# Optimization experiments

Measured on AMD Instinct MI355X. Metric: run time of the kernel, lower is better.

The kernel has to match this reference:

```python
import jax, jax.numpy as jnp
from jax import lax
import numpy as np

N, D, H, ENT = 32768, 16, 128, 50000


def setup_inputs() -> dict:
    key = jax.random.key(0)
    ks = jax.random.split(key, 10)
    s = 0.05  # weight scale to keep tanh/sigmoid in active range
    return {
        "ent_table": jax.random.normal(ks[0], (ENT, H), jnp.float32) * s,
        "op_table": jax.random.normal(ks[1], (5, H), jnp.float32) * s,
        "non_table": jax.random.normal(ks[2], (1, H), jnp.float32) * s,
        "Wm": jax.random.normal(ks[3], (H, 3 * H), jnp.float32) * s,
        "bm": jnp.zeros((H,), jnp.float32),
        "Wg": jax.random.normal(ks[4], (H, 3 * H), jnp.float32) * s,
        "bg": jnp.zeros((H,), jnp.float32),
        "ops_idx": jax.random.randint(ks[5], (N, D), 0, 4, jnp.int32),
        "ents_idx": jax.random.randint(ks[6], (N, D + 1), 0, ENT, jnp.int32),
        "left_idx": jax.random.randint(ks[7], (N,), 0, ENT, jnp.int32),
    }


def reference(ent_table, op_table, non_table, Wm, bm, Wg, bg, ops_idx, ents_idx, left_idx):
    # Merge module (dropout in eval mode = identity):
    #   tanh(Linear([node, t1, t2])) * sigmoid(Linear_g([node, t1, t2]))
    def merge(node, t1, t2):
        x = jnp.concatenate([node, t1, t2], axis=-1)  # [N, 3H]
        return jnp.tanh(x @ Wm.T + bm) * jax.nn.sigmoid(x @ Wg.T + bg)

    op_e = op_table[ops_idx]        # [N, D, H]
    ent_e = ent_table[ents_idx]     # [N, D+1, H]

    # Right-leaning prefix tree: acc starts at deepest entity, merge upward.
    acc0 = ent_e[:, -1]             # [N, H]
    # scan over depth, from innermost (i = D-1) to outermost (i = 0)
    xs = (jnp.flip(op_e, axis=1).transpose(1, 0, 2),          # [D, N, H]
          jnp.flip(ent_e[:, :-1], axis=1).transpose(1, 0, 2))  # [D, N, H]

    def step(acc, inp):
        o, e = inp
        return merge(o, e, acc), None

    acc, _ = lax.scan(step, acc0, xs)

    eq_e = jnp.broadcast_to(op_table[4], acc.shape)  # '=' embedding, [N, H]
    left_e = ent_table[left_idx]                     # [N, H]
    score = merge(eq_e, left_e, acc)                 # [N, H]

    # all_score = cat(per-formula scores, non_embed)  -> [N+1, H]
    return jnp.concatenate([score, non_table], axis=0)
```

## Files before the change

kernel.cpp:

```cpp
#include <hip/hip_runtime.h>
#include <hip/hip_bf16.h>
#include <hip/hip_fp16.h>

#define NROWS 32768
#define HH 128
#define ENTN 50000

typedef _Float16 f16x8 __attribute__((ext_vector_type(8)));
typedef __fp16 fp16x2 __attribute__((ext_vector_type(2)));
typedef float f32x4 __attribute__((ext_vector_type(4)));
typedef float f32x16 __attribute__((ext_vector_type(16)));

#define OFF_PEB 0
#define OFF_EB  25600000
#define OFF_WF  38400000
#define OFF_PEF (OFF_WF + 65536)
#define OFF_POPK (OFF_PEF + 65536)

#define KM 2.8853901f
#define KG (-1.4426950f)
#define RSTR 272
#define HALF (32 * RSTR)

#if defined(__has_builtin)
#if __has_builtin(__builtin_amdgcn_exp2f)
#define FEXP2(x) __builtin_amdgcn_exp2f(x)
#endif
#endif
#ifndef FEXP2
__device__ __forceinline__ float __fexp2_asm(float x) {
    float r; asm("v_exp_f32 %0, %1" : "=v"(r) : "v"(x)); return r;
}
#define FEXP2(x) __fexp2_asm(x)
#endif

__device__ __forceinline__ unsigned pk2(float a, float b) {
    fp16x2 h = __builtin_amdgcn_cvt_pkrtz(a, b);
    unsigned u; __builtin_memcpy(&u, &h, 4); return u;
}
__device__ __forceinline__ unsigned pk2rtn(float a, float b) {
    _Float16 lo = (_Float16)a, hi = (_Float16)b;
    unsigned short ul, uh;
    __builtin_memcpy(&ul, &lo, 2); __builtin_memcpy(&uh, &hi, 2);
    return (unsigned)ul | ((unsigned)uh << 16);
}

__global__ void prep_kernel(const float* __restrict__ ent_table,
                            const float* __restrict__ op_table,
                            const float* __restrict__ non_table,
                            const float* __restrict__ Wm, const float* __restrict__ bm,
                            const float* __restrict__ Wg, const float* __restrict__ bg,
                            char* __restrict__ ws, float* __restrict__ out) {
    int idx = blockIdx.x * blockDim.x + threadIdx.x;
    if (idx < 800000) {
        _Float16* EB = (_Float16*)(ws + OFF_EB);
        int base = idx * 8;
        const float4* s = (const float4*)(ent_table + base);
        float4 v0 = s[0], v1 = s[1];
        float xv[8] = {v0.x, v0.y, v0.z, v0.w, v1.x, v1.y, v1.z, v1.w};
        _Float16 h8[8];
        #pragma unroll
        for (int j = 0; j < 8; ++j) h8[j] = (_Float16)xv[j];
        *(f16x8*)(EB + base) = *(f16x8*)h8;
    } else if (idx < 832768) {
        int e = idx - 800000;
        int jj = e & 7, l = (e >> 3) & 63, kt = (e >> 9) & 7, jb = e >> 12;
        int j = jb * 32 + (l & 31);
        int c = j >> 1, p = j & 1;
        int k = kt * 16 + (l >> 5) * 8 + jj;
        const float* Wrow = p ? (Wg + (size_t)c * 384) : (Wm + (size_t)c * 384);
        ((_Float16*)(ws + OFF_WF))[e] = (_Float16)(Wrow[256 + k] * (p ? KG : KM));
    } else if (idx < 865536) {
        int e = idx - 832768;
        int jj = e & 7, l = (e >> 3) & 63, kt = (e >> 9) & 3, jb = e >> 11;
        int j = jb * 16 + (l & 15);
        int c = j >> 1, p = j & 1;
        int k = kt * 32 + (l >> 4) * 8 + jj;
        const float* Wrow = p ? (Wg + (size_t)c * 384) : (Wm + (size_t)c * 384);
        ((_Float16*)(ws + OFF_PEF))[e] = (_Float16)Wrow[128 + k];
    } else if (idx < 866176) {
        int t2 = idx - 865536;
        int pr = t2 & 1, q = (t2 >> 1) & 3, h = (t2 >> 3) & 1, jb = (t2 >> 4) & 7, o = t2 >> 7;
        int j0 = jb * 32 + 8 * q + 4 * h + 2 * pr;
        int c = j0 >> 1;
        float sm = bm[c], sg = bg[c];
        const float* Wrm = Wm + (size_t)c * 384;
        const float* Wrg = Wg + (size_t)c * 384;
        for (int i = 0; i < 128; ++i) {
            float ov = op_table[o * HH + i];
            sm += ov * Wrm[i];
            sg += ov * Wrg[i];
        }
        ((unsigned*)(ws + OFF_POPK))[t2] = pk2rtn(sm * KM, sg * KG);
    } else if (idx < 866304) {
        int j = idx - 866176;
        out[(size_t)NROWS * HH + j] = non_table[j];
    }
}

__global__ __launch_bounds__(256, 4)
void pe_kernel(char* __restrict__ ws) {
    const char* EBc = ws + OFF_EB;
    const f16x8* PEF = (const f16x8*)(ws + OFF_PEF);
    char* PEB = ws + OFF_PEB;
    int tid = threadIdx.x, w = tid >> 6, l = tid & 63, lr = l & 15, lg = (l >> 4) & 3;
    int e0 = blockIdx.x * 32;

    f16x8 WB[4][4];
    #pragma unroll
    for (int u = 0; u < 4; ++u)
        #pragma unroll
        for (int kt = 0; kt < 4; ++kt)
            WB[u][kt] = PEF[((4 * w + u) * 4 + kt) * 64 + l];

    f32x4 C[2][4];
    #pragma unroll
    for (int rt = 0; rt < 2; ++rt)
        #pragma unroll
        for (int u = 0; u < 4; ++u) C[rt][u] = (f32x4){0.f, 0.f, 0.f, 0.f};

    #pragma unroll
    for (int kt = 0; kt < 4; ++kt) {
        #pragma unroll
        for (int rt = 0; rt < 2; ++rt) {
            int e = e0 + rt * 16 + lr;
            if (e >= ENTN) e = ENTN - 1;
            f16x8 A = *(const f16x8*)(EBc + (size_t)e * 256 + kt * 64 + lg * 16);
            #pragma unroll
            for (int u = 0; u < 4; ++u)
                C[rt][u] = __builtin_amdgcn_mfma_f32_16x16x32_f16(WB[u][kt], A, C[rt][u], 0, 0, 0);
        }
    }
    #pragma unroll
    for (int rt = 0; rt < 2; ++rt) {
        int e = e0 + rt * 16 + lr;
        if (e < ENTN) {
            #pragma unroll
            for (int u = 0; u < 4; ++u) {
                int c = (4 * w + u) * 8 + 2 * lg;
                int jb2 = c >> 4, rem = c & 15;
                int q = rem >> 2, h2 = (rem >> 1) & 1;
                uint2 st;
                st.x = pk2(C[rt][u][0] * KM, C[rt][u][1] * KG);
                st.y = pk2(C[rt][u][2] * KM, C[rt][u][3] * KG);
                *(uint2*)(PEB + (size_t)e * 512 + jb2 * 64 + h2 * 32 + q * 8) = st;
            }
        }
    }
}

__global__ __launch_bounds__(512, 4)
void chain_kernel(const float* __restrict__ ent_table,
                  const int* __restrict__ ops_idx,
                  const int* __restrict__ ents_idx,
                  const int* __restrict__ left_idx,
                  const char* __restrict__ ws, float* __restrict__ out) {
    __shared__ char Abuf[2 * HALF];
    __shared__ unsigned eo[17 * 32];
    __shared__ unsigned popk[640];

    const char* PEBc = ws + OFF_PEB;
    const f16x8* WFp = (const f16x8*)(ws + OFF_WF);
    const unsigned* POPKg = (const unsigned*)(ws + OFF_POPK);

    int tid = threadIdx.x;
    int jb = tid >> 6, l = tid & 63, r = l & 31, h = l >> 5;
    int row0 = blockIdx.x * 32;

    for (int i = tid; i < 544; i += 512) {
        int t = i >> 5, rr = i & 31;
        unsigned e, o;
        if (t < 16) {
            e = ents_idx[(row0 + rr) * 17 + 15 - t];
            o = ops_idx[(row0 + rr) * 16 + 15 - t];
        } else {
            e = left_idx[row0 + rr];
            o = 4;
        }
        eo[i] = (e << 9) | o;
    }
    for (int i = tid; i < 640; i += 512) popk[i] = POPKg[i];

    f16x8 WH[8];
    #pragma unroll
    for (int kt = 0; kt < 8; ++kt)
        WH[kt] = WFp[(jb * 8 + kt) * 64 + l];

    {
        int rr = tid >> 4, sub = tid & 15;
        int e = ents_idx[(row0 + rr) * 17 + 16];
        const float4* src = (const float4*)(ent_table + (size_t)e * HH + sub * 8);
        float4 v0 = src[0], v1 = src[1];
        uint4 d;
        d.x = pk2(v0.x, v0.y); d.y = pk2(v0.z, v0.w);
        d.z = pk2(v1.x, v1.y); d.w = pk2(v1.z, v1.w);
        *(uint4*)(Abuf + rr * RSTR + sub * 16) = d;
    }
    __syncthreads();

    int rb = r * RSTR + h * 16;
    int wb = r * RSTR + jb * 32 + h * 4;
    const char* pebBase = PEBc + jb * 64 + h * 32;
    const char* popkB = (const char*)popk + jb * 64 + h * 32;
    const unsigned* eoB = eo + r;

    unsigned va = eoB[0];
    uint4 pa0 = *(const uint4*)(pebBase + (va & 0xFFFFFE00u));
    uint4 pa1 = *(const uint4*)(pebBase + (va & 0xFFFFFE00u) + 16);

#define DO_STEP(T, RD, WR, FINAL)                                               \
    {                                                                           \
        uint4 npa0, npa1; unsigned nva = 0;                                     \
        if (!(FINAL)) {                                                         \
            nva = eoB[((T) + 1) * 32];                                          \
            npa0 = *(const uint4*)(pebBase + (nva & 0xFFFFFE00u));              \
            npa1 = *(const uint4*)(pebBase + (nva & 0xFFFFFE00u) + 16);         \
        }                                                                       \
        const char* pq = popkB + (va & 7u) * 512;                               \
        uint4 po0 = *(const uint4*)(pq);                                        \
        uint4 po1 = *(const uint4*)(pq + 16);                                   \
        unsigned pe_u[8] = {pa0.x, pa0.y, pa0.z, pa0.w, pa1.x, pa1.y, pa1.z, pa1.w}; \
        unsigned po_u[8] = {po0.x, po0.y, po0.z, po0.w, po1.x, po1.y, po1.z, po1.w}; \
        f32x16 C;                                                               \
        _Pragma("unroll")                                                       \
        for (int q = 0; q < 4; ++q)                                             \
            _Pragma("unroll")                                                   \
            for (int pr = 0; pr < 2; ++pr) {                                    \
                int u = q * 2 + pr;                                             \
                __half2 sa = *(const __half2*)&pe_u[u];                         \
                __half2 sb = *(const __half2*)&po_u[u];                         \
                __half2 s = __hadd2(sa, sb);                                    \
                C[4 * q + 2 * pr] = __low2float(s);                             \
                C[4 * q + 2 * pr + 1] = __high2float(s);                        \
            }                                                                   \
        _Pragma("unroll")                                                       \
        for (int kt = 0; kt < 8; ++kt) {                                        \
            f16x8 A = *(const f16x8*)(Abuf + rb + (RD) + kt * 32);              \
            C = __builtin_amdgcn_mfma_f32_32x32x16_f16(WH[kt], A, C, 0, 0, 0);  \
        }                                                                       \
        _Pragma("unroll")                                                       \
        for (int q = 0; q < 4; ++q) {                                           \
            float ov[2];                                                        \
            _Pragma("unroll")                                                   \
            for (int pr = 0; pr < 2; ++pr) {                                    \
                float m = C[4 * q + 2 * pr];                                    \
                float g = C[4 * q + 2 * pr + 1];                                \
                float em = FEXP2(m), eg = FEXP2(g);                             \
                ov[pr] = (em - 1.f) * __builtin_amdgcn_rcpf((em + 1.f) * (1.f + eg)); \
            }                                                                   \
            if (FINAL) {                                                        \
                *(float2*)(out + (size_t)(row0 + r) * HH + jb * 16 + 4 * q + 2 * h) \
                    = make_float2(ov[0], ov[1]);                                \
            } else {                                                            \
                *(unsigned*)(Abuf + wb + (WR) + q * 8) = pk2(ov[0], ov[1]);     \
            }                                                                   \
        }                                                                       \
        __syncthreads();                                                        \
        if (!(FINAL)) { pa0 = npa0; pa1 = npa1; va = nva; }                     \
    }

    for (int tb = 0; tb < 8; ++tb) {
        int t0 = 2 * tb;
        DO_STEP(t0, 0, HALF, 0)
        DO_STEP(t0 + 1, HALF, 0, 0)
    }
    DO_STEP(16, 0, HALF, 1)
#undef DO_STEP
}

extern "C" void kernel_launch(void* const* d_in, const int* in_sizes, int n_in,
                              void* d_out, int out_size, void* d_ws, size_t ws_size,
                              hipStream_t stream) {
    const float* ent_table = (const float*)d_in[0];
    const float* op_table  = (const float*)d_in[1];
    const float* non_table = (const float*)d_in[2];
    const float* Wm        = (const float*)d_in[3];
    const float* bm        = (const float*)d_in[4];
    const float* Wg        = (const float*)d_in[5];
    const float* bg        = (const float*)d_in[6];
    const int* ops_idx     = (const int*)d_in[7];
    const int* ents_idx    = (const int*)d_in[8];
    const int* left_idx    = (const int*)d_in[9];
    float* out = (float*)d_out;
    char* ws = (char*)d_ws;

    prep_kernel<<<3384, 256, 0, stream>>>(ent_table, op_table, non_table,
                                          Wm, bm, Wg, bg, ws, out);
    pe_kernel<<<1563, 256, 0, stream>>>(ws);
    chain_kernel<<<NROWS / 32, 512, 0, stream>>>(ent_table, ops_idx, ents_idx,
                                                 left_idx, ws, out);
}
```

Measured before the change: 101.7 us.

## Fuse entity projection into chain kernel instead of precomputing all entities

Removes the pe_kernel that projected all 50000 entity embeddings through the middle weight slice. The chain kernel now stages each step's gathered fp16 entity rows in shared memory and runs eight extra MFMAs per step against a register-held scaled weight slice. This avoids a full-table matmul and a 25.6MB intermediate write and read. In exchange it doubles the chain's per-step MFMA work and adds shared-memory traffic on the serial critical path.

```diff
diff --git a/kernel.cpp b/kernel.cpp
--- a/kernel.cpp
+++ b/kernel.cpp
@@ -8,14 +8,12 @@
 
 typedef _Float16 f16x8 __attribute__((ext_vector_type(8)));
 typedef __fp16 fp16x2 __attribute__((ext_vector_type(2)));
-typedef float f32x4 __attribute__((ext_vector_type(4)));
 typedef float f32x16 __attribute__((ext_vector_type(16)));
 
-#define OFF_PEB 0
-#define OFF_EB  25600000
-#define OFF_WF  38400000
-#define OFF_PEF (OFF_WF + 65536)
-#define OFF_POPK (OFF_PEF + 65536)
+#define OFF_EB   0
+#define OFF_WF   12800000
+#define OFF_WEF  (OFF_WF + 65536)
+#define OFF_POPK (OFF_WEF + 65536)
 
 #define KM 2.8853901f
 #define KG (-1.4426950f)
@@ -72,12 +70,12 @@
         ((_Float16*)(ws + OFF_WF))[e] = (_Float16)(Wrow[256 + k] * (p ? KG : KM));
     } else if (idx < 865536) {
         int e = idx - 832768;
-        int jj = e & 7, l = (e >> 3) & 63, kt = (e >> 9) & 3, jb = e >> 11;
-        int j = jb * 16 + (l & 15);
+        int jj = e & 7, l = (e >> 3) & 63, kt = (e >> 9) & 7, jb = e >> 12;
+        int j = jb * 32 + (l & 31);
         int c = j >> 1, p = j & 1;
-        int k = kt * 32 + (l >> 4) * 8 + jj;
+        int k = kt * 16 + (l >> 5) * 8 + jj;
         const float* Wrow = p ? (Wg + (size_t)c * 384) : (Wm + (size_t)c * 384);
-        ((_Float16*)(ws + OFF_PEF))[e] = (_Float16)Wrow[128 + k];
+        ((_Float16*)(ws + OFF_WEF))[e] = (_Float16)(Wrow[128 + k] * (p ? KG : KM));
     } else if (idx < 866176) {
         int t2 = idx - 865536;
         int pr = t2 & 1, q = (t2 >> 1) & 3, h = (t2 >> 3) & 1, jb = (t2 >> 4) & 7, o = t2 >> 7;
@@ -98,57 +96,6 @@
     }
 }
 
-__global__ __launch_bounds__(256, 4)
-void pe_kernel(char* __restrict__ ws) {
-    const char* EBc = ws + OFF_EB;
-    const f16x8* PEF = (const f16x8*)(ws + OFF_PEF);
-    char* PEB = ws + OFF_PEB;
-    int tid = threadIdx.x, w = tid >> 6, l = tid & 63, lr = l & 15, lg = (l >> 4) & 3;
-    int e0 = blockIdx.x * 32;
-
-    f16x8 WB[4][4];
-    #pragma unroll
-    for (int u = 0; u < 4; ++u)
-        #pragma unroll
-        for (int kt = 0; kt < 4; ++kt)
-            WB[u][kt] = PEF[((4 * w + u) * 4 + kt) * 64 + l];
-
-    f32x4 C[2][4];
-    #pragma unroll
-    for (int rt = 0; rt < 2; ++rt)
-        #pragma unroll
-        for (int u = 0; u < 4; ++u) C[rt][u] = (f32x4){0.f, 0.f, 0.f, 0.f};
-
-    #pragma unroll
-    for (int kt = 0; kt < 4; ++kt) {
-        #pragma unroll
-        for (int rt = 0; rt < 2; ++rt) {
-            int e = e0 + rt * 16 + lr;
-            if (e >= ENTN) e = ENTN - 1;
-            f16x8 A = *(const f16x8*)(EBc + (size_t)e * 256 + kt * 64 + lg * 16);
-            #pragma unroll
-            for (int u = 0; u < 4; ++u)
-                C[rt][u] = __builtin_amdgcn_mfma_f32_16x16x32_f16(WB[u][kt], A, C[rt][u], 0, 0, 0);
-        }
-    }
-    #pragma unroll
-    for (int rt = 0; rt < 2; ++rt) {
-        int e = e0 + rt * 16 + lr;
-        if (e < ENTN) {
-            #pragma unroll
-            for (int u = 0; u < 4; ++u) {
-                int c = (4 * w + u) * 8 + 2 * lg;
-                int jb2 = c >> 4, rem = c & 15;
-                int q = rem >> 2, h2 = (rem >> 1) & 1;
-                uint2 st;
-                st.x = pk2(C[rt][u][0] * KM, C[rt][u][1] * KG);
-                st.y = pk2(C[rt][u][2] * KM, C[rt][u][3] * KG);
-                *(uint2*)(PEB + (size_t)e * 512 + jb2 * 64 + h2 * 32 + q * 8) = st;
-            }
-        }
-    }
-}
-
 __global__ __launch_bounds__(512, 4)
 void chain_kernel(const float* __restrict__ ent_table,
                   const int* __restrict__ ops_idx,
@@ -156,11 +103,13 @@
                   const int* __restrict__ left_idx,
                   const char* __restrict__ ws, float* __restrict__ out) {
     __shared__ char Abuf[2 * HALF];
+    __shared__ char Ebuf[2 * HALF];
     __shared__ unsigned eo[17 * 32];
     __shared__ unsigned popk[640];
 
-    const char* PEBc = ws + OFF_PEB;
+    const char* EBc = ws + OFF_EB;
     const f16x8* WFp = (const f16x8*)(ws + OFF_WF);
+    const f16x8* WEFp = (const f16x8*)(ws + OFF_WEF);
     const unsigned* POPKg = (const unsigned*)(ws + OFF_POPK);
 
     int tid = threadIdx.x;
@@ -179,65 +128,70 @@
         }
         eo[i] = (e << 9) | o;
     }
-    for (int i = tid; i < 640; i += 512) popk[i] = POPKg[i];
-
-    f16x8 WH[8];
+    if (tid < 160) ((uint4*)popk)[tid] = ((const uint4*)POPKg)[tid];
+
+    f16x8 WH[8], WE[8];
     #pragma unroll
-    for (int kt = 0; kt < 8; ++kt)
+    for (int kt = 0; kt < 8; ++kt) {
         WH[kt] = WFp[(jb * 8 + kt) * 64 + l];
-
+        WE[kt] = WEFp[(jb * 8 + kt) * 64 + l];
+    }
+
+    int srr = tid >> 4, ssub = tid & 15;
     {
-        int rr = tid >> 4, sub = tid & 15;
-        int e = ents_idx[(row0 + rr) * 17 + 16];
-        const float4* src = (const float4*)(ent_table + (size_t)e * HH + sub * 8);
+        int e = ents_idx[(row0 + srr) * 17 + 16];
+        const float4* src = (const float4*)(ent_table + (size_t)e * HH + ssub * 8);
         float4 v0 = src[0], v1 = src[1];
         uint4 d;
         d.x = pk2(v0.x, v0.y); d.y = pk2(v0.z, v0.w);
         d.z = pk2(v1.x, v1.y); d.w = pk2(v1.z, v1.w);
-        *(uint4*)(Abuf + rr * RSTR + sub * 16) = d;
+        *(uint4*)(Abuf + srr * RSTR + ssub * 16) = d;
+        int e0e = ents_idx[(row0 + srr) * 17 + 15];
+        *(uint4*)(Ebuf + srr * RSTR + ssub * 16) =
+            *(const uint4*)(EBc + (size_t)e0e * 256 + ssub * 16);
     }
     __syncthreads();
 
     int rb = r * RSTR + h * 16;
     int wb = r * RSTR + jb * 32 + h * 4;
-    const char* pebBase = PEBc + jb * 64 + h * 32;
     const char* popkB = (const char*)popk + jb * 64 + h * 32;
     const unsigned* eoB = eo + r;
 
-    unsigned va = eoB[0];
-    uint4 pa0 = *(const uint4*)(pebBase + (va & 0xFFFFFE00u));
-    uint4 pa1 = *(const uint4*)(pebBase + (va & 0xFFFFFE00u) + 16);
-
 #define DO_STEP(T, RD, WR, FINAL)                                               \
     {                                                                           \
-        uint4 npa0, npa1; unsigned nva = 0;                                     \
-        if (!(FINAL)) {                                                         \
-            nva = eoB[((T) + 1) * 32];                                          \
-            npa0 = *(const uint4*)(pebBase + (nva & 0xFFFFFE00u));              \
-            npa1 = *(const uint4*)(pebBase + (nva & 0xFFFFFE00u) + 16);         \
-        }                                                                       \
+        uint4 sev;                                                              \
+        if (!(FINAL)) {      \
+            unsigned se = eo[((T) + 1) * 32 + srr] >> 9;                        \
+            sev = *(const uint4*)(EBc + (size_t)se * 256 + ssub * 16);          \
+        }                                                                       \
+        unsigned va = eoB[(T) * 32];                                            \
         const char* pq = popkB + (va & 7u) * 512;                               \
         uint4 po0 = *(const uint4*)(pq);                                        \
         uint4 po1 = *(const uint4*)(pq + 16);                                   \
-        unsigned pe_u[8] = {pa0.x, pa0.y, pa0.z, pa0.w, pa1.x, pa1.y, pa1.z, pa1.w}; \
-        unsigned po_u[8] = {po0.x, po0.y, po0.z, po0.w, po1.x, po1.y, po1.z, po1.w}; \
+        unsigned po_u[8] = {po0.x, po0.y, po0.z, po0.w,                         \
+                            po1.x, po1.y, po1.z, po1.w};                        \
         f32x16 C;                                                               \
         _Pragma("unroll")                                                       \
         for (int q = 0; q < 4; ++q)                                             \
             _Pragma("unroll")                                                   \
             for (int pr = 0; pr < 2; ++pr) {                                    \
                 int u = q * 2 + pr;                                             \
-                __half2 sa = *(const __half2*)&pe_u[u];                         \
                 __half2 sb = *(const __half2*)&po_u[u];                         \
-                __half2 s = __hadd2(sa, sb);                                    \
-                C[4 * q + 2 * pr] = __low2float(s);                             \
-                C[4 * q + 2 * pr + 1] = __high2float(s);                        \
+                C[4 * q + 2 * pr] = __low2float(sb);                            \
+                C[4 * q + 2 * pr + 1] = __high2float(sb);                       \
             }                                                                   \
         _Pragma("unroll")                                                       \
         for (int kt = 0; kt < 8; ++kt) {                                        \
             f16x8 A = *(const f16x8*)(Abuf + rb + (RD) + kt * 32);              \
             C = __builtin_amdgcn_mfma_f32_32x32x16_f16(WH[kt], A, C, 0, 0, 0);  \
         }                                                                       \
+        _Pragma("unroll")                                                       \
+        for (int kt = 0; kt < 8; ++kt) {                                        \
+            f16x8 A = *(const f16x8*)(Ebuf + rb + (RD) + kt * 32);              \
+            C = __builtin_amdgcn_mfma_f32_32x32x16_f16(WE[kt], A, C, 0, 0, 0);  \
+        }                                                                       \
+        if (!(FINAL))                                                           \
+            *(uint4*)(Ebuf + (WR) + srr * RSTR + ssub * 16) = sev;              \
         _Pragma("unroll")                                                       \
         for (int q = 0; q < 4; ++q) {                                           \
             float ov[2];                                                        \
@@ -256,7 +210,6 @@
             }                                                                   \
         }                                                                       \
         __syncthreads();                                                        \
-        if (!(FINAL)) { pa0 = npa0; pa1 = npa1; va = nva; }                     \
     }
 
     for (int tb = 0; tb < 8; ++tb) {
@@ -286,7 +239,6 @@
 
     prep_kernel<<<3384, 256, 0, stream>>>(ent_table, op_table, non_table,
                                           Wm, bm, Wg, bg, ws, out);
-    pe_kernel<<<1563, 256, 0, stream>>>(ws);
     chain_kernel<<<NROWS / 32, 512, 0, stream>>>(ent_table, ops_idx, ents_idx,
                                                  left_idx, ws, out);
 }
```

Result: no change. 103.6 us (+1.8%).
